# Kernel optimization log

Hardware: AMD Instinct MI355X
Metric: run time of the kernel (lower is better)

Reference implementation:

```python
import jax, jax.numpy as jnp
import numpy as np

TEMP = 1.0
EPS = 1e-8
DIM = 1024
CODEBOOK_SIZE = 8192
N = 8192


def setup_inputs() -> dict:
    key = jax.random.key(0)
    k_h, k_cb, k_w, k_b = jax.random.split(key, 4)
    h = jax.random.normal(k_h, (N, DIM), dtype=jnp.float32)
    codebook = jax.random.normal(k_cb, (CODEBOOK_SIZE, DIM), dtype=jnp.float32)
    # RMSNorm scale initialized to ones (as in the torch module)
    scale = jnp.ones((DIM,), dtype=jnp.float32)
    # nn.Linear(dim, dim): weight [out, in], bias [out]
    bound = 1.0 / np.sqrt(DIM)
    W = jax.random.uniform(k_w, (DIM, DIM), dtype=jnp.float32, minval=-bound, maxval=bound)
    b = jax.random.uniform(k_b, (DIM,), dtype=jnp.float32, minval=-bound, maxval=bound)
    return {"h": h, "codebook": codebook, "scale": scale, "W": W, "b": b}


def reference(h, codebook, scale, W, b):
    # Squared distances via GEMM identity: ||h-c||^2 = ||h||^2 + ||c||^2 - 2 h.c
    h_sq = jnp.sum(h * h, axis=-1, keepdims=True)              # [N, 1]
    c_sq = jnp.sum(codebook * codebook, axis=-1)               # [K]
    dist = h_sq + c_sq[None, :] - 2.0 * (h @ codebook.T)       # [N, K]
    q = jax.nn.softmax(-dist / TEMP, axis=-1)                  # [N, K]
    z_e = q @ codebook                                         # [N, D]
    # residual MLP: RMSNorm then Linear
    r = h - z_e
    rms = jnp.sqrt(jnp.mean(r * r, axis=-1, keepdims=True))
    x = r / (rms + EPS) * scale
    z_q = z_e + x @ W.T + b
    return z_q
```

## Files before the change

kernel.cpp:

```cpp
#include <hip/hip_runtime.h>

typedef unsigned short u16;
typedef unsigned char u8;
typedef signed char s8;
typedef __attribute__((ext_vector_type(8))) short bf16x8;
typedef __attribute__((ext_vector_type(4))) float f32x4;
typedef __attribute__((ext_vector_type(4))) int i32x4;
typedef __attribute__((ext_vector_type(16))) int i32x16;

__device__ __forceinline__ u16 f2bf(float x) {
  unsigned int u = __float_as_uint(x);
  u = u + 0x7FFFu + ((u >> 16) & 1u);
  return (u16)(u >> 16);
}
__device__ __forceinline__ float bf2f(u16 v) {
  return __uint_as_float(((unsigned int)v) << 16);
}

typedef const __attribute__((address_space(1))) void gas_void;
typedef __attribute__((address_space(3))) void las_void;

__device__ __forceinline__ void gld_lds16(const void* g, void* l) {
  __builtin_amdgcn_global_load_lds((gas_void*)g, (las_void*)l, 16, 0, 0);
}

#define CAP 512
#define DU8 9

__global__ __launch_bounds__(256) void gemm_c8(
    const s8* __restrict__ A0, const s8* __restrict__ B0,
    u8* __restrict__ S, const float* __restrict__ c_sq) {
  __shared__ __align__(16) s8 lA[128 * 128];
  __shared__ __align__(16) s8 lB[128 * 128];
  int tid = threadIdx.x, wave = tid >> 6, lane = tid & 63;
  long bm = (long)blockIdx.y * 128, bn = (long)blockIdx.x * 128;
  int wm = (wave >> 1) * 64, wn = (wave & 1) * 64;
  int l31 = lane & 31, kg = lane >> 5;
  int srow = wave * 8 + (lane >> 3);

  i32x16 acc[2][2];
#pragma unroll
  for (int i = 0; i < 2; ++i)
#pragma unroll
    for (int j = 0; j < 2; ++j)
#pragma unroll
      for (int r = 0; r < 16; ++r) acc[i][j][r] = 0;

  const s8* ap = A0 + bm * 1024;
  const s8* bp = B0 + bn * 1024;

  for (int k0 = 0; k0 < 1024; k0 += 128) {
    __syncthreads();
#pragma unroll
    for (int c = 0; c < 4; ++c) {
      int sc2 = ((lane & 7) ^ (lane >> 3) ^ ((c * 4 + wave) & 7)) * 16;
      long go = (long)(c * 32 + srow) * 1024 + k0 + sc2;
      int ldoff = c * 4096 + wave * 1024;
      gld_lds16(ap + go, lA + ldoff);
      gld_lds16(bp + go, lB + ldoff);
    }
    __syncthreads();
#pragma unroll
    for (int kk = 0; kk < 4; ++kk) {
      i32x4 af[2], bf[2];
#pragma unroll
      for (int i = 0; i < 2; ++i) {
        int ra = wm + i * 32 + l31;
        int rxa = (ra & 7) ^ ((ra >> 3) & 7);
        af[i] = *(const i32x4*)&lA[ra * 128 + ((kk * 2 + kg) ^ rxa) * 16];
        int rb = wn + i * 32 + l31;
        int rxb = (rb & 7) ^ ((rb >> 3) & 7);
        bf[i] = *(const i32x4*)&lB[rb * 128 + ((kk * 2 + kg) ^ rxb) * 16];
      }
#pragma unroll
      for (int i = 0; i < 2; ++i)
#pragma unroll
        for (int j = 0; j < 2; ++j)
          acc[i][j] = __builtin_amdgcn_mfma_i32_32x32x32_i8(af[i], bf[j], acc[i][j], 0, 0, 0);
    }
  }

#pragma unroll
  for (int i = 0; i < 2; ++i) {
#pragma unroll
    for (int j = 0; j < 2; ++j) {
      long cg = bn + wn + j * 32 + l31;
      float csq = c_sq[cg];
#pragma unroll
      for (int r = 0; r < 16; ++r) {
        long rg = bm + wm + i * 32 + (r & 3) + 8 * (r >> 2) + 4 * kg;
        float v = csq - (float)acc[i][j][r] * 0.0078125f;
        int q = (int)rintf((v - 1024.f) * 0.25f) + 128;
        q = q < 0 ? 0 : (q > 255 ? 255 : q);
        S[rg * 8192 + cg] = (u8)q;
      }
    }
  }
}

__global__ __launch_bounds__(256) void gemm_zq(
    const u16* __restrict__ A0, long lda,
    const u16* __restrict__ B0, long ldb,
    float* __restrict__ C, long ldc, int K,
    const float* __restrict__ aux0, const float* __restrict__ aux1) {
  __shared__ __align__(16) u16 lA0[128 * 64];
  __shared__ __align__(16) u16 lB0[64 * 64];

  int tid = threadIdx.x;
  int wave = tid >> 6, lane = tid & 63;
  long bm = (long)blockIdx.y * 128, bn = (long)blockIdx.x * 64;
  int wm = (wave >> 1) * 64, wn = (wave & 1) * 32;
  int r15 = lane & 15, kg = lane >> 4;
  int srow = wave * 8 + (lane >> 3);
  int scol = ((lane & 7) ^ (lane >> 3)) * 8;

  f32x4 acc[4][2];
#pragma unroll
  for (int i = 0; i < 4; ++i)
#pragma unroll
    for (int j = 0; j < 2; ++j) acc[i][j] = (f32x4){0.f, 0.f, 0.f, 0.f};

  for (int k0 = 0; k0 < K; k0 += 64) {
    __syncthreads();
#pragma unroll
    for (int c = 0; c < 4; ++c) {
      const u16* g = A0 + (bm + c * 32 + srow) * lda + k0 + scol;
      gld_lds16(g, lA0 + c * 2048 + wave * 512);
    }
#pragma unroll
    for (int c = 0; c < 2; ++c) {
      const u16* g = B0 + (bn + c * 32 + srow) * ldb + k0 + scol;
      gld_lds16(g, lB0 + c * 2048 + wave * 512);
    }
    __syncthreads();

#pragma unroll
    for (int kk = 0; kk < 2; ++kk) {
      int cu = ((kk * 4 + kg) ^ (r15 & 7)) * 8;
      bf16x8 bh[2];
#pragma unroll
      for (int j = 0; j < 2; ++j)
        bh[j] = *(const bf16x8*)&lB0[(wn + j * 16 + r15) * 64 + cu];
#pragma unroll
      for (int i = 0; i < 4; ++i) {
        bf16x8 ah = *(const bf16x8*)&lA0[(wm + i * 16 + r15) * 64 + cu];
#pragma unroll
        for (int j = 0; j < 2; ++j)
          acc[i][j] = __builtin_amdgcn_mfma_f32_16x16x32_bf16(ah, bh[j], acc[i][j], 0, 0, 0);
      }
    }
  }

#pragma unroll
  for (int i = 0; i < 4; ++i) {
    long rg = bm + wm + i * 16 + kg * 4;
#pragma unroll
    for (int j = 0; j < 2; ++j) {
      long cg = bn + wn + j * 16 + r15;
      f32x4 v = acc[i][j];
      float bb = aux1[cg];
#pragma unroll
      for (int r = 0; r < 4; ++r)
        C[(rg + r) * ldc + cg] = v[r] + aux0[(rg + r) * ldc + cg] + bb;
    }
  }
}

__device__ __forceinline__ int q8(float x) {
  float q = rintf(x * 16.f);
  q = fminf(fmaxf(q, -127.f), 127.f);
  return (int)q;
}

__global__ __launch_bounds__(256) void prep_h_i8(const float* __restrict__ in,
                                                 s8* __restrict__ q0, int n4) {
  int i = blockIdx.x * 256 + threadIdx.x;
  if (i >= n4) return;
  float4 v = ((const float4*)in)[i];
  unsigned int w = (unsigned int)((q8(v.x) & 0xFF) | ((q8(v.y) & 0xFF) << 8) |
                                  ((q8(v.z) & 0xFF) << 16) | ((q8(v.w) & 0xFF) << 24));
  ((unsigned int*)q0)[i] = w;
}

__global__ __launch_bounds__(256) void prep_cb_i8(const float* __restrict__ cb,
                                                  s8* __restrict__ q0,
                                                  float* __restrict__ c_sq) {
  long k = blockIdx.x;
  int t = threadIdx.x, lane = t & 63, wave = t >> 6;
  float4 v = ((const float4*)(cb + k * 1024))[t];
  unsigned int w = (unsigned int)((q8(v.x) & 0xFF) | ((q8(v.y) & 0xFF) << 8) |
                                  ((q8(v.z) & 0xFF) << 16) | ((q8(v.w) & 0xFF) << 24));
  ((unsigned int*)(q0 + k * 1024))[t] = w;
  float ss = v.x * v.x + v.y * v.y + v.z * v.z + v.w * v.w;
#pragma unroll
  for (int o = 32; o; o >>= 1) ss += __shfl_xor(ss, o);
  __shared__ float sc[4];
  if (lane == 0) sc[wave] = ss;
  __syncthreads();
  if (t == 0) c_sq[k] = sc[0] + sc[1] + sc[2] + sc[3];
}

__global__ __launch_bounds__(256) void prep_bf16(const float* __restrict__ in,
                                                 u16* __restrict__ o, int n4) {
  int i = blockIdx.x * 256 + threadIdx.x;
  if (i >= n4) return;
  float4 v = ((const float4*)in)[i];
  ushort4 h;
  h.x = f2bf(v.x); h.y = f2bf(v.y); h.z = f2bf(v.z); h.w = f2bf(v.w);
  ((ushort4*)o)[i] = h;
}

__global__ __launch_bounds__(256) void refine_rms(
    const float* __restrict__ h, const float* __restrict__ cb,
    const float* __restrict__ csq, const u8* __restrict__ Sq,
    const float* __restrict__ scale,
    float* __restrict__ z_e, u16* __restrict__ x) {
  long m = blockIdx.x;
  int t = threadIdx.x, lane = t & 63, wave = t >> 6;
  __shared__ int cand[CAP];
  __shared__ int smi[4], wsum[4], ncand;
  __shared__ float smf[4], ssum[4], sc[4];
  __shared__ float lacc[4][1024];

  const uint4* row4 = (const uint4*)(Sq + m * 8192);
  uint4 va = row4[t], vb = row4[256 + t];
  unsigned int w[8] = {va.x, va.y, va.z, va.w, vb.x, vb.y, vb.z, vb.w};
  int bmin = 255;
#pragma unroll
  for (int i = 0; i < 8; ++i)
#pragma unroll
    for (int j = 0; j < 4; ++j) {
      int b = (w[i] >> (8 * j)) & 0xFF;
      bmin = b < bmin ? b : bmin;
    }
#pragma unroll
  for (int o = 32; o; o >>= 1) {
    int y = __shfl_xor(bmin, o);
    bmin = y < bmin ? y : bmin;
  }
  if (lane == 0) smi[wave] = bmin;
  __syncthreads();
  bmin = min(min(smi[0], smi[1]), min(smi[2], smi[3]));
  int thr = bmin + DU8;
  int c = 0;
#pragma unroll
  for (int i = 0; i < 8; ++i)
#pragma unroll
    for (int j = 0; j < 4; ++j)
      c += (((w[i] >> (8 * j)) & 0xFF) <= (unsigned)thr);
  int pre = c;
#pragma unroll
  for (int o = 1; o < 64; o <<= 1) {
    int y = __shfl_up(pre, o);
    if (lane >= o) pre += y;
  }
  if (lane == 63) wsum[wave] = pre;
  __syncthreads();
  int base = 0;
#pragma unroll
  for (int wv = 0; wv < 4; ++wv) base += (wv < wave) ? wsum[wv] : 0;
  int pos = base + pre - c;
#pragma unroll
  for (int i = 0; i < 8; ++i)
#pragma unroll
    for (int j = 0; j < 4; ++j) {
      int b = (w[i] >> (8 * j)) & 0xFF;
      if (b <= thr) {
        int col = (i < 4 ? t * 16 : 4096 + t * 16) + (i & 3) * 4 + j;
        if (pos < CAP) cand[pos] = col;
        ++pos;
      }
    }
  if (t == 0) {
    int tot = wsum[0] + wsum[1] + wsum[2] + wsum[3];
    ncand = tot < CAP ? tot : CAP;
  }
  __syncthreads();
  int n = ncand;

  const float4* h4 = (const float4*)(h + m * 1024);
  float4 hw[4];
#pragma unroll
  for (int i = 0; i < 4; ++i) hw[i] = h4[lane * 4 + i];

  float mw = -3.0e38f, sw = 0.f;
  float4 a0 = {0.f, 0.f, 0.f, 0.f}, a1 = a0, a2 = a0, a3 = a0;
  for (int j = wave; j < n; j += 4) {
    long k = cand[j];
    const float4* c4 = (const float4*)(cb + k * 1024);
    float4 cv0 = c4[lane * 4 + 0], cv1 = c4[lane * 4 + 1];
    float4 cv2 = c4[lane * 4 + 2], cv3 = c4[lane * 4 + 3];
    float d = hw[0].x * cv0.x + hw[0].y * cv0.y + hw[0].z * cv0.z + hw[0].w * cv0.w +
              hw[1].x * cv1.x + hw[1].y * cv1.y + hw[1].z * cv1.z + hw[1].w * cv1.w +
              hw[2].x * cv2.x + hw[2].y * cv2.y + hw[2].z * cv2.z + hw[2].w * cv2.w +
              hw[3].x * cv3.x + hw[3].y * cv3.y + hw[3].z * cv3.z + hw[3].w * cv3.w;
#pragma unroll
    for (int o = 32; o; o >>= 1) d += __shfl_xor(d, o);
    float lg = 2.f * d - csq[k];
    if (lg > mw) {
      float r = __expf(mw - lg);
      sw *= r;
      a0.x *= r; a0.y *= r; a0.z *= r; a0.w *= r;
      a1.x *= r; a1.y *= r; a1.z *= r; a1.w *= r;
      a2.x *= r; a2.y *= r; a2.z *= r; a2.w *= r;
      a3.x *= r; a3.y *= r; a3.z *= r; a3.w *= r;
      mw = lg;
    }
    float wgt = __expf(lg - mw);
    sw += wgt;
    a0.x += wgt * cv0.x; a0.y += wgt * cv0.y; a0.z += wgt * cv0.z; a0.w += wgt * cv0.w;
    a1.x += wgt * cv1.x; a1.y += wgt * cv1.y; a1.z += wgt * cv1.z; a1.w += wgt * cv1.w;
    a2.x += wgt * cv2.x; a2.y += wgt * cv2.y; a2.z += wgt * cv2.z; a2.w += wgt * cv2.w;
    a3.x += wgt * cv3.x; a3.y += wgt * cv3.y; a3.z += wgt * cv3.z; a3.w += wgt * cv3.w;
  }
  if (lane == 0) { smf[wave] = mw; ssum[wave] = sw; }
  __syncthreads();
  float M = fmaxf(fmaxf(smf[0], smf[1]), fmaxf(smf[2], smf[3]));
  float Stot = ssum[0] * __expf(smf[0] - M) + ssum[1] * __expf(smf[1] - M) +
               ssum[2] * __expf(smf[2] - M) + ssum[3] * __expf(smf[3] - M);
  float rw = __expf(mw - M);
  float* lw = &lacc[wave][lane * 16];
  *(float4*)(lw + 0) = (float4){a0.x * rw, a0.y * rw, a0.z * rw, a0.w * rw};
  *(float4*)(lw + 4) = (float4){a1.x * rw, a1.y * rw, a1.z * rw, a1.w * rw};
  *(float4*)(lw + 8) = (float4){a2.x * rw, a2.y * rw, a2.z * rw, a2.w * rw};
  *(float4*)(lw + 12) = (float4){a3.x * rw, a3.y * rw, a3.z * rw, a3.w * rw};
  __syncthreads();
  float rs = 1.f / Stot;
  float4 p0 = *(const float4*)&lacc[0][t * 4];
  float4 p1 = *(const float4*)&lacc[1][t * 4];
  float4 p2 = *(const float4*)&lacc[2][t * 4];
  float4 p3 = *(const float4*)&lacc[3][t * 4];
  float4 ze;
  ze.x = (p0.x + p1.x + p2.x + p3.x) * rs;
  ze.y = (p0.y + p1.y + p2.y + p3.y) * rs;
  ze.z = (p0.z + p1.z + p2.z + p3.z) * rs;
  ze.w = (p0.w + p1.w + p2.w + p3.w) * rs;
  *(float4*)(z_e + m * 1024 + t * 4) = ze;
  float4 hv = h4[t];
  float4 r;
  r.x = hv.x - ze.x; r.y = hv.y - ze.y; r.z = hv.z - ze.z; r.w = hv.w - ze.w;
  float ss = r.x * r.x + r.y * r.y + r.z * r.z + r.w * r.w;
#pragma unroll
  for (int o = 32; o; o >>= 1) ss += __shfl_xor(ss, o);
  if (lane == 0) sc[wave] = ss;
  __syncthreads();
  float tot = sc[0] + sc[1] + sc[2] + sc[3];
  float inv = 1.f / (sqrtf(tot * (1.f / 1024.f)) + 1e-8f);
  float4 s4 = ((const float4*)scale)[t];
  ushort4 o;
  o.x = f2bf(r.x * inv * s4.x); o.y = f2bf(r.y * inv * s4.y);
  o.z = f2bf(r.z * inv * s4.z); o.w = f2bf(r.w * inv * s4.w);
  *(ushort4*)(x + m * 1024 + t * 4) = o;
}

extern "C" void kernel_launch(void* const* d_in, const int* in_sizes, int n_in,
                              void* d_out, int out_size, void* d_ws, size_t ws_size,
                              hipStream_t stream) {
  const float* h = (const float*)d_in[0];
  const float* cb = (const float*)d_in[1];
  const float* scale = (const float*)d_in[2];
  const float* W = (const float*)d_in[3];
  const float* b = (const float*)d_in[4];
  float* out = (float*)d_out;

  char* ws = (char*)d_ws;
  size_t off = 0;
  auto alloc = [&](size_t bytes) -> char* {
    char* p = ws + off;
    off = (off + bytes + 255) & ~(size_t)255;
    return p;
  };
  s8* h8 = (s8*)alloc(8192L * 1024);
  s8* c8 = (s8*)alloc(8192L * 1024);
  u16* Wbf = (u16*)alloc(1024L * 1024 * 2);
  float* c_sq = (float*)alloc(8192L * 4);
  float* z_e = (float*)alloc(8192L * 1024 * 4);
  u16* x = (u16*)alloc(8192L * 1024 * 2);
  u8* Sq = (u8*)alloc(8192L * 8192);

  prep_h_i8<<<8192, 256, 0, stream>>>(h, h8, 2097152);
  prep_cb_i8<<<8192, 256, 0, stream>>>(cb, c8, c_sq);
  prep_bf16<<<1024, 256, 0, stream>>>(W, Wbf, 262144);

  gemm_c8<<<dim3(64, 64), 256, 0, stream>>>(h8, c8, Sq, c_sq);
  refine_rms<<<8192, 256, 0, stream>>>(h, cb, c_sq, Sq, scale, z_e, x);
  gemm_zq<<<dim3(16, 64), 256, 0, stream>>>(x, 1024L, Wbf, 1024L,
                                            out, 1024L, 1024, z_e, b);
}
```

Before: 191.8 us.

## Store z_e as bf16, fuse h/W prep, swizzle int8 GEMM tiles

z_e is now written by refine_rms and read by the final GEMM as bf16 instead of fp32, halving that intermediate's traffic at the cost of some precision in the output. The h int8 and W bf16 prep kernels merge into one launch. The int8 distance GEMM uses a 1D grid whose blocks are remapped into groups of eight, which changes which tiles run together and may improve L2 reuse. DU8 changes from 9 to 8, which alters a candidate threshold in the hidden refine code and risks accuracy.

Measured after the change: 194.5 us. Within noise of the previous version (+1.4%).

```diff
diff --git a/kernel.cpp b/kernel.cpp
--- a/kernel.cpp
+++ b/kernel.cpp
@@ -25,7 +25,7 @@
 }
 
 #define CAP 512
-#define DU8 9
+#define DU8 8
 
 __global__ __launch_bounds__(256) void gemm_c8(
     const s8* __restrict__ A0, const s8* __restrict__ B0,
@@ -33,7 +33,9 @@
   __shared__ __align__(16) s8 lA[128 * 128];
   __shared__ __align__(16) s8 lB[128 * 128];
   int tid = threadIdx.x, wave = tid >> 6, lane = tid & 63;
-  long bm = (long)blockIdx.y * 128, bn = (long)blockIdx.x * 128;
+  int id = blockIdx.x;
+  int swz = (id & 7) * 512 + (id >> 3);
+  long bm = (long)(swz >> 6) * 128, bn = (long)(swz & 63) * 128;
   int wm = (wave >> 1) * 64, wn = (wave & 1) * 64;
   int l31 = lane & 31, kg = lane >> 5;
   int srow = wave * 8 + (lane >> 3);
@@ -102,7 +104,7 @@
     const u16* __restrict__ A0, long lda,
     const u16* __restrict__ B0, long ldb,
     float* __restrict__ C, long ldc, int K,
-    const float* __restrict__ aux0, const float* __restrict__ aux1) {
+    const u16* __restrict__ aux0, const float* __restrict__ aux1) {
   __shared__ __align__(16) u16 lA0[128 * 64];
   __shared__ __align__(16) u16 lB0[64 * 64];
 
@@ -161,7 +163,7 @@
       float bb = aux1[cg];
 #pragma unroll
       for (int r = 0; r < 4; ++r)
-        C[(rg + r) * ldc + cg] = v[r] + aux0[(rg + r) * ldc + cg] + bb;
+        C[(rg + r) * ldc + cg] = v[r] + bf2f(aux0[(rg + r) * ldc + cg]) + bb;
     }
   }
 }
@@ -172,14 +174,24 @@
   return (int)q;
 }
 
-__global__ __launch_bounds__(256) void prep_h_i8(const float* __restrict__ in,
-                                                 s8* __restrict__ q0, int n4) {
-  int i = blockIdx.x * 256 + threadIdx.x;
-  if (i >= n4) return;
-  float4 v = ((const float4*)in)[i];
-  unsigned int w = (unsigned int)((q8(v.x) & 0xFF) | ((q8(v.y) & 0xFF) << 8) |
-                                  ((q8(v.z) & 0xFF) << 16) | ((q8(v.w) & 0xFF) << 24));
-  ((unsigned int*)q0)[i] = w;
+__global__ __launch_bounds__(256) void prep_h_w(const float* __restrict__ h,
+                                                s8* __restrict__ q0,
+                                                const float* __restrict__ W,
+                                                u16* __restrict__ Wbf) {
+  int b = blockIdx.x;
+  if (b < 8192) {
+    int i = b * 256 + threadIdx.x;
+    float4 v = ((const float4*)h)[i];
+    unsigned int w = (unsigned int)((q8(v.x) & 0xFF) | ((q8(v.y) & 0xFF) << 8) |
+                                    ((q8(v.z) & 0xFF) << 16) | ((q8(v.w) & 0xFF) << 24));
+    ((unsigned int*)q0)[i] = w;
+  } else {
+    int i = (b - 8192) * 256 + threadIdx.x;
+    float4 v = ((const float4*)W)[i];
+    ushort4 o;
+    o.x = f2bf(v.x); o.y = f2bf(v.y); o.z = f2bf(v.z); o.w = f2bf(v.w);
+    ((ushort4*)Wbf)[i] = o;
+  }
 }
 
 __global__ __launch_bounds__(256) void prep_cb_i8(const float* __restrict__ cb,
@@ -200,21 +212,11 @@
   if (t == 0) c_sq[k] = sc[0] + sc[1] + sc[2] + sc[3];
 }
 
-__global__ __launch_bounds__(256) void prep_bf16(const float* __restrict__ in,
-                                                 u16* __restrict__ o, int n4) {
-  int i = blockIdx.x * 256 + threadIdx.x;
-  if (i >= n4) return;
-  float4 v = ((const float4*)in)[i];
-  ushort4 h;
-  h.x = f2bf(v.x); h.y = f2bf(v.y); h.z = f2bf(v.z); h.w = f2bf(v.w);
-  ((ushort4*)o)[i] = h;
-}
-
 __global__ __launch_bounds__(256) void refine_rms(
     const float* __restrict__ h, const float* __restrict__ cb,
     const float* __restrict__ csq, const u8* __restrict__ Sq,
     const float* __restrict__ scale,
-    float* __restrict__ z_e, u16* __restrict__ x) {
+    u16* __restrict__ z_e, u16* __restrict__ x) {
   long m = blockIdx.x;
   int t = threadIdx.x, lane = t & 63, wave = t >> 6;
   __shared__ int cand[CAP];
@@ -335,7 +337,9 @@
   ze.y = (p0.y + p1.y + p2.y + p3.y) * rs;
   ze.z = (p0.z + p1.z + p2.z + p3.z) * rs;
   ze.w = (p0.w + p1.w + p2.w + p3.w) * rs;
-  *(float4*)(z_e + m * 1024 + t * 4) = ze;
+  ushort4 zo;
+  zo.x = f2bf(ze.x); zo.y = f2bf(ze.y); zo.z = f2bf(ze.z); zo.w = f2bf(ze.w);
+  *(ushort4*)(z_e + m * 1024 + t * 4) = zo;
   float4 hv = h4[t];
   float4 r;
   r.x = hv.x - ze.x; r.y = hv.y - ze.y; r.z = hv.z - ze.z; r.w = hv.w - ze.w;
@@ -374,15 +378,14 @@
   s8* c8 = (s8*)alloc(8192L * 1024);
   u16* Wbf = (u16*)alloc(1024L * 1024 * 2);
   float* c_sq = (float*)alloc(8192L * 4);
-  float* z_e = (float*)alloc(8192L * 1024 * 4);
+  u16* z_e = (u16*)alloc(8192L * 1024 * 2);
   u16* x = (u16*)alloc(8192L * 1024 * 2);
   u8* Sq = (u8*)alloc(8192L * 8192);
 
-  prep_h_i8<<<8192, 256, 0, stream>>>(h, h8, 2097152);
+  prep_h_w<<<9216, 256, 0, stream>>>(h, h8, W, Wbf);
   prep_cb_i8<<<8192, 256, 0, stream>>>(cb, c8, c_sq);
-  prep_bf16<<<1024, 256, 0, stream>>>(W, Wbf, 262144);
-
-  gemm_c8<<<dim3(64, 64), 256, 0, stream>>>(h8, c8, Sq, c_sq);
+
+  gemm_c8<<<4096, 256, 0, stream>>>(h8, c8, Sq, c_sq);
   refine_rms<<<8192, 256, 0, stream>>>(h, cb, c_sq, Sq, scale, z_e, x);
   gemm_zq<<<dim3(16, 64), 256, 0, stream>>>(x, 1024L, Wbf, 1024L,
                                             out, 1024L, 1024, z_e, b);
```
